# Kernel tuning notes

Measured on AMD Instinct MI355X. Metric: run time of the kernel, lower is better.

Reference implementation:

```python
import jax, jax.numpy as jnp
import numpy as np

# Static config (KITTI PointPillars-style)
B, PB, N = 4, 12000, 32          # batches, pillars per batch, max points per pillar
P = B * PB
NX, NY, NZ, F = 432, 496, 1, 64  # grid and PFN output channels
PX, PY, PZ = 0.16, 0.16, 4.0     # pillar size
XO, YO, ZO = 0.08, -39.6, -1.0   # pillar-center offsets = size/2 + range_min
EPS = 1e-3                        # BatchNorm eps


def setup_inputs() -> dict:
    key = jax.random.key(0)
    ks = jax.random.split(key, 10)
    pillars = jax.random.normal(ks[0], (P, N, 8), jnp.float32)
    # unique BEV cells per batch so the scatter (torch advanced-index assign) is well-defined
    rng = np.random.default_rng(0)
    cs = []
    for b in range(B):
        lin = rng.choice(NY * NX, size=PB, replace=False)
        cs.append(np.stack([np.full(PB, b), np.zeros(PB, np.int64), lin // NX, lin % NX], 1))
    coords = jnp.asarray(np.concatenate(cs, 0), jnp.int32)  # [P,4] = (batch, z, y, x)
    num_points = jax.random.randint(ks[1], (P,), 1, N + 1, jnp.int32)

    def bn_stats(k, f):  # rows: gamma, beta, running_mean, running_var
        k1, k2, k3, k4 = jax.random.split(k, 4)
        return jnp.stack([jax.random.uniform(k1, (f,), jnp.float32, 0.8, 1.2),
                          jax.random.normal(k2, (f,)) * 0.1,
                          jax.random.normal(k3, (f,)) * 0.1,
                          jax.random.uniform(k4, (f,), jnp.float32, 0.5, 1.5)])

    return {
        'pillars': pillars,
        'w1': jax.random.normal(ks[2], (10, F), jnp.float32) * 0.1,
        'bn1': bn_stats(ks[4], F),
        'w2': jax.random.normal(ks[3], (8, F), jnp.float32) * 0.1,
        'bn2': bn_stats(ks[5], F),
        'wf1': jax.random.normal(ks[6], (F,), jnp.float32) * 0.1,
        'wf2': jax.random.normal(ks[7], (F,), jnp.float32) * 0.1,
        'fbn1': bn_stats(ks[8], 1)[:, 0],
        'fbn2': bn_stats(ks[9], 1)[:, 0],
        'coords': coords,
        'num_points': num_points,
    }


def _bn(x, stats):  # x [..., F], stats [4, F] or [4]
    g, b, m, v = stats[0], stats[1], stats[2], stats[3]
    return (x - m) * (g * jax.lax.rsqrt(v + EPS)) + b


def _pfn(x, w, stats):  # x [P, N, C] -> [P, F]: linear + BN(eval) + relu + max over points
    h = jnp.einsum('pnc,cf->pnf', x, w)
    return jax.nn.relu(_bn(h, stats)).max(axis=1)


def _forward(pillars, w1, bn1, w2, bn2, wf1, wf2, fbn1, fbn2, coords, num_points):
    xyz = pillars[:, :, :3]                                   # [P, N, 3]
    # relative xyz to cluster mean
    mean_xyz = xyz.sum(axis=1, keepdims=True) / num_points.astype(jnp.float32)[:, None, None]
    to_cluster = xyz - mean_xyz
    # relative xyz to pillar center; coords cols = (batch, z, y, x)
    cf = coords.astype(jnp.float32)
    center = jnp.stack([cf[:, 3] * PX + XO, cf[:, 2] * PY + YO, cf[:, 1] * PZ + ZO], axis=-1)
    to_center = xyz - center[:, None, :]

    pv_in = jnp.concatenate([pillars[:, :, :4], to_cluster, to_center], axis=-1)  # [P, N, 10]
    f1 = _pfn(pv_in, w1, bn1)      # [P, F] geometric stream
    f2 = _pfn(pillars, w2, bn2)    # [P, F] seg stream (full 8 channels)

    # scatter pillar features to BEV canvas: idx = z + y*nx + x (nz=1 -> z=0)
    lin = coords[:, 1] + coords[:, 2] * NX + coords[:, 3]
    b_idx = coords[:, 0]
    bev1 = jnp.zeros((B, NZ * NY * NX, F), jnp.float32).at[b_idx, lin].set(f1)
    bev2 = jnp.zeros((B, NZ * NY * NX, F), jnp.float32).at[b_idx, lin].set(f2)
    x1 = bev1.reshape(B, NY, NX, F).transpose(0, 3, 1, 2)  # [B, F, NY, NX]
    x2 = bev2.reshape(B, NY, NX, F).transpose(0, 3, 1, 2)

    # attentional fusion: 1x1 conv (no bias) + BN2d(1) per stream, softmax over the 2 weights
    s1 = _bn(jnp.einsum('bfyx,f->byx', x1, wf1), fbn1)
    s2 = _bn(jnp.einsum('bfyx,f->byx', x2, wf2), fbn2)
    aw = jax.nn.softmax(jnp.stack([s1, s2], axis=1), axis=1)  # [B, 2, NY, NX]
    return x1 * aw[:, 0:1] + x2 * aw[:, 1:2]


def reference(pillars, w1, bn1, w2, bn2, wf1, wf2, fbn1, fbn2, coords, num_points):
    return _forward(pillars, w1, bn1, w2, bn2, wf1, wf2, fbn1, fbn2, coords, num_points)
```

## Files before the change

### kernel.cpp

```cpp
#include <hip/hip_runtime.h>
#include <math.h>

#define NXC 432
#define NYC 496
#define CELLS (NYC * NXC)
#define BATCH 4
#define PTOT 48000
#define EPSC 1e-3f
#define TCELLS 128

typedef float f4v    __attribute__((ext_vector_type(4)));
typedef float f32x16 __attribute__((ext_vector_type(16)));
typedef __bf16 bf16x8 __attribute__((ext_vector_type(8)));

__global__ __launch_bounds__(256) void pfe_kernel(
    const float* __restrict__ pillars, const float* __restrict__ w1,
    const float* __restrict__ bn1, const float* __restrict__ w2,
    const float* __restrict__ bn2, const float* __restrict__ wf1,
    const float* __restrict__ wf2, const float* __restrict__ fbn1,
    const float* __restrict__ fbn2, const int* __restrict__ coords,
    const int* __restrict__ num_points, float* __restrict__ comb,
    int* __restrict__ map)
{
    const int tid  = threadIdx.x;
    const int lane = tid & 63;
    const int ln   = lane & 31;
    const bool hi  = lane >= 32;
    const int p = __builtin_amdgcn_readfirstlane(blockIdx.x * 4 + (tid >> 6));
    const float* __restrict__ pl = pillars + (size_t)p * 256;

    const f4v v0 = *(const f4v*)(pl + ln * 8);
    const f4v v1 = *(const f4v*)(pl + ln * 8 + 4);

    float sx = v0.x, sy = v0.y, sz = v0.z;
#pragma unroll
    for (int off = 1; off <= 16; off <<= 1) {
        sx += __shfl_xor(sx, off);
        sy += __shfl_xor(sy, off);
        sz += __shfl_xor(sz, off);
    }
    const float inv_np = 1.0f / (float)num_points[p];
    const float mxm = sx * inv_np, mym = sy * inv_np, mzm = sz * inv_np;

    const int c1 = coords[p * 4 + 1], c2 = coords[p * 4 + 2], c3 = coords[p * 4 + 3];
    const float cx = c3 * 0.16f + 0.08f;
    const float cy = c2 * 0.16f + (-39.6f);
    const float cz = c1 * 4.0f  + (-1.0f);

    float AXc[2], AYc[2], AZc[2], AIc[2], C0c[2];
    float Bc[2][8], C2c[2], WF1c[2], WF2c[2];
#pragma unroll
    for (int i = 0; i < 2; ++i) {
        const int c = ln + i * 32;
        const float s1 = bn1[c] * rsqrtf(bn1[192 + c] + EPSC);
        const float be1 = bn1[64 + c], bm1 = bn1[128 + c];
        const float w10 = w1[c],       w11 = w1[64 + c],  w12 = w1[128 + c];
        const float w13 = w1[192 + c], w14 = w1[256 + c], w15 = w1[320 + c];
        const float w16 = w1[384 + c], w17 = w1[448 + c], w18 = w1[512 + c];
        const float w19 = w1[576 + c];
        AXc[i] = (w10 + w14 + w17) * s1;
        AYc[i] = (w11 + w15 + w18) * s1;
        AZc[i] = (w12 + w16 + w19) * s1;
        AIc[i] = w13 * s1;
        C0c[i] = be1 - bm1 * s1
               - (mxm * w14 + mym * w15 + mzm * w16) * s1
               - (cx * w17 + cy * w18 + cz * w19) * s1;

        const float s2 = bn2[c] * rsqrtf(bn2[192 + c] + EPSC);
#pragma unroll
        for (int k = 0; k < 8; ++k) Bc[i][k] = w2[k * 64 + c] * s2;
        C2c[i] = bn2[64 + c] - bn2[128 + c] * s2;
        WF1c[i] = wf1[c];
        WF2c[i] = wf2[c];
    }

    const float fe0 = v0.x, fe1 = v0.y, fe2 = v0.z, fe3 = v0.w;
    const float fe4 = v1.x, fe5 = v1.y, fe6 = v1.z, fe7 = v1.w;
    bf16x8 a;
    {
        const float f[8] = {fe0, fe1, fe2, fe3, fe4, fe5, fe6, fe7};
#pragma unroll
        for (int e = 0; e < 8; ++e) {
            const __bf16 h = (__bf16)f[e];
            const __bf16 l = (__bf16)(f[e] - (float)h);
            a[e] = hi ? l : h;
        }
    }

    const bf16x8 b0 = {(__bf16)AXc[0], (__bf16)AYc[0], (__bf16)AZc[0], (__bf16)AIc[0],
                       (__bf16)0.f, (__bf16)0.f, (__bf16)0.f, (__bf16)0.f};
    const bf16x8 b1 = {(__bf16)AXc[1], (__bf16)AYc[1], (__bf16)AZc[1], (__bf16)AIc[1],
                       (__bf16)0.f, (__bf16)0.f, (__bf16)0.f, (__bf16)0.f};
    const bf16x8 b2 = {(__bf16)Bc[0][0], (__bf16)Bc[0][1], (__bf16)Bc[0][2], (__bf16)Bc[0][3],
                       (__bf16)Bc[0][4], (__bf16)Bc[0][5], (__bf16)Bc[0][6], (__bf16)Bc[0][7]};
    const bf16x8 b3 = {(__bf16)Bc[1][0], (__bf16)Bc[1][1], (__bf16)Bc[1][2], (__bf16)Bc[1][3],
                       (__bf16)Bc[1][4], (__bf16)Bc[1][5], (__bf16)Bc[1][6], (__bf16)Bc[1][7]};

    f32x16 d0 = {0.f}, d1 = {0.f}, d2 = {0.f}, d3 = {0.f};
    d0 = __builtin_amdgcn_mfma_f32_32x32x16_bf16(a, b0, d0, 0, 0, 0);
    d1 = __builtin_amdgcn_mfma_f32_32x32x16_bf16(a, b1, d1, 0, 0, 0);
    d2 = __builtin_amdgcn_mfma_f32_32x32x16_bf16(a, b2, d2, 0, 0, 0);
    d3 = __builtin_amdgcn_mfma_f32_32x32x16_bf16(a, b3, d3, 0, 0, 0);

    float m0 = d0[0], m1 = d1[0], m2 = d2[0], m3 = d3[0];
#pragma unroll
    for (int r = 1; r < 16; ++r) {
        m0 = fmaxf(m0, d0[r]); m1 = fmaxf(m1, d1[r]);
        m2 = fmaxf(m2, d2[r]); m3 = fmaxf(m3, d3[r]);
    }
    m0 = fmaxf(m0, __shfl_xor(m0, 32));
    m1 = fmaxf(m1, __shfl_xor(m1, 32));
    m2 = fmaxf(m2, __shfl_xor(m2, 32));
    m3 = fmaxf(m3, __shfl_xor(m3, 32));

    const float f1A = fmaxf(m0 + C0c[0], 0.f);
    const float f1B = fmaxf(m1 + C0c[1], 0.f);
    const float f2A = fmaxf(m2 + C2c[0], 0.f);
    const float f2B = fmaxf(m3 + C2c[1], 0.f);

    float dd1 = f1A * WF1c[0] + f1B * WF1c[1];
    float dd2 = f2A * WF2c[0] + f2B * WF2c[1];
#pragma unroll
    for (int off = 1; off <= 16; off <<= 1) {
        dd1 += __shfl_xor(dd1, off);
        dd2 += __shfl_xor(dd2, off);
    }
    const float sc1 = (dd1 - fbn1[2]) * (fbn1[0] * rsqrtf(fbn1[3] + EPSC)) + fbn1[1];
    const float sc2 = (dd2 - fbn2[2]) * (fbn2[0] * rsqrtf(fbn2[3] + EPSC)) + fbn2[1];
    const float a0 = 1.0f / (1.0f + expf(sc2 - sc1));

    if (!hi) {
        comb[p * 64 + ln]      = fmaf(f1A - f2A, a0, f2A);
        comb[p * 64 + 32 + ln] = fmaf(f1B - f2B, a0, f2B);
    }
    if (lane == 0) {
        const int lin = c1 + c2 * NXC + c3;
        map[coords[p * 4 + 0] * CELLS + lin] = p;
    }
}

__global__ __launch_bounds__(256) void emit_kernel(
    const int* __restrict__ map, const float* __restrict__ comb,
    float* __restrict__ out)
{
    __shared__ float lds[64 * 132];
    const int t = threadIdx.x;
    const int gbase = blockIdx.x * TCELLS;

    {
        const int c = t >> 1;
        const int h = (t & 1) * 32;
        const int m = map[gbase + c];
        float* dst = lds + h * 132 + c;
        if (m >= 0) {
            const float* src = comb + (size_t)m * 64 + h;
#pragma unroll
            for (int j = 0; j < 8; j++) {
                const float4 v = *(const float4*)(src + j * 4);
                dst[(j * 4 + 0) * 132] = v.x;
                dst[(j * 4 + 1) * 132] = v.y;
                dst[(j * 4 + 2) * 132] = v.z;
                dst[(j * 4 + 3) * 132] = v.w;
            }
        } else {
#pragma unroll
            for (int j = 0; j < 32; j++) dst[j * 132] = 0.f;
        }
    }
    __syncthreads();

    const int b = gbase / CELLS;
    const int L = gbase - b * CELLS;
    float* obase = out + (size_t)(b * 64) * CELLS + L;
#pragma unroll
    for (int r = 0; r < 8; r++) {
        const int idx = r * 256 + t;
        const int f = idx >> 5;
        const int g = idx & 31;
        const f4v v = *(const f4v*)(lds + f * 132 + g * 4);
        __builtin_nontemporal_store(v, (f4v*)(obase + (size_t)f * CELLS + g * 4));
    }
}

extern "C" void kernel_launch(void* const* d_in, const int* in_sizes, int n_in,
                              void* d_out, int out_size, void* d_ws, size_t ws_size,
                              hipStream_t stream) {
    const float* pillars = (const float*)d_in[0];
    const float* w1      = (const float*)d_in[1];
    const float* bn1     = (const float*)d_in[2];
    const float* w2      = (const float*)d_in[3];
    const float* bn2     = (const float*)d_in[4];
    const float* wf1     = (const float*)d_in[5];
    const float* wf2     = (const float*)d_in[6];
    const float* fbn1    = (const float*)d_in[7];
    const float* fbn2    = (const float*)d_in[8];
    const int*   coords  = (const int*)d_in[9];
    const int*   nump    = (const int*)d_in[10];
    float* out = (float*)d_out;

    int*   map  = (int*)d_ws;
    float* comb = (float*)((char*)d_ws + (size_t)BATCH * CELLS * 4);

    (void)hipMemsetAsync(map, 0xFF, (size_t)BATCH * CELLS * 4, stream);
    pfe_kernel<<<PTOT / 4, 256, 0, stream>>>(pillars, w1, bn1, w2, bn2,
                                             wf1, wf2, fbn1, fbn2,
                                             coords, nump, comb, map);
    emit_kernel<<<(BATCH * CELLS) / TCELLS, 256, 0, stream>>>(map, comb, out);
}
```

Baseline: 89.16 us.

## Precompute folded BN weights once in a table kernel; skip zero-fill LDS writes in emit

A new single-block kernel folds the BatchNorm scale and shift into the PFN weights once per call and stores them as packed bf16 MFMA operands plus float constants in a workspace table. Each pillar wave then loads from this table instead of recomputing rsqrt and many weight products per pillar. The emit kernel stops writing zeros into LDS for empty cells and instead records cell occupancy in shared memory, masking values at store time. This adds an extra kernel launch and a dependency on the table in exchange for less per-pillar arithmetic and fewer LDS writes.

Result: faster. 83.88 us (-5.9%).

```diff
diff --git a/kernel.cpp b/kernel.cpp
--- a/kernel.cpp
+++ b/kernel.cpp
@@ -8,19 +8,71 @@
 #define PTOT 48000
 #define EPSC 1e-3f
 #define TCELLS 128
-
+#define TBL_STRIDE 20
+
+typedef float f2v    __attribute__((ext_vector_type(2)));
 typedef float f4v    __attribute__((ext_vector_type(4)));
 typedef float f32x16 __attribute__((ext_vector_type(16)));
 typedef __bf16 bf16x8 __attribute__((ext_vector_type(8)));
+typedef unsigned int u32x4 __attribute__((ext_vector_type(4)));
+
+__device__ __forceinline__ unsigned int pk_bf16(float a, float b) {
+    __bf16 ha = (__bf16)a, hb = (__bf16)b;
+    unsigned short ua = __builtin_bit_cast(unsigned short, ha);
+    unsigned short ub = __builtin_bit_cast(unsigned short, hb);
+    return ((unsigned int)ub << 16) | ua;
+}
+
+__global__ __launch_bounds__(64) void fold_kernel(
+    const float* __restrict__ w1, const float* __restrict__ bn1,
+    const float* __restrict__ w2, const float* __restrict__ bn2,
+    const float* __restrict__ wf1, const float* __restrict__ wf2,
+    unsigned int* __restrict__ tbl)
+{
+    const int c = threadIdx.x;
+    const float s1 = bn1[c] * rsqrtf(bn1[192 + c] + EPSC);
+    const float w10 = w1[c],       w11 = w1[64 + c],  w12 = w1[128 + c];
+    const float w13 = w1[192 + c], w14 = w1[256 + c], w15 = w1[320 + c];
+    const float w16 = w1[384 + c], w17 = w1[448 + c], w18 = w1[512 + c];
+    const float w19 = w1[576 + c];
+    const float AX = (w10 + w14 + w17) * s1;
+    const float AY = (w11 + w15 + w18) * s1;
+    const float AZ = (w12 + w16 + w19) * s1;
+    const float AI = w13 * s1;
+
+    const float s2 = bn2[c] * rsqrtf(bn2[192 + c] + EPSC);
+    float B[8];
+#pragma unroll
+    for (int k = 0; k < 8; ++k) B[k] = w2[k * 64 + c] * s2;
+
+    unsigned int* t = tbl + c * TBL_STRIDE;
+    t[0] = pk_bf16(AX, AY);
+    t[1] = pk_bf16(AZ, AI);
+    t[2] = 0u;
+    t[3] = 0u;
+    t[4] = pk_bf16(B[0], B[1]);
+    t[5] = pk_bf16(B[2], B[3]);
+    t[6] = pk_bf16(B[4], B[5]);
+    t[7] = pk_bf16(B[6], B[7]);
+    float* tf = (float*)t;
+    tf[8]  = bn1[64 + c] - bn1[128 + c] * s1;
+    tf[9]  = w14 * s1;
+    tf[10] = w15 * s1;
+    tf[11] = w16 * s1;
+    tf[12] = w17 * s1;
+    tf[13] = w18 * s1;
+    tf[14] = w19 * s1;
+    tf[15] = bn2[64 + c] - bn2[128 + c] * s2;
+    tf[16] = wf1[c];
+    tf[17] = wf2[c];
+    tf[18] = 0.f; tf[19] = 0.f;
+}
 
 __global__ __launch_bounds__(256) void pfe_kernel(
-    const float* __restrict__ pillars, const float* __restrict__ w1,
-    const float* __restrict__ bn1, const float* __restrict__ w2,
-    const float* __restrict__ bn2, const float* __restrict__ wf1,
-    const float* __restrict__ wf2, const float* __restrict__ fbn1,
-    const float* __restrict__ fbn2, const int* __restrict__ coords,
-    const int* __restrict__ num_points, float* __restrict__ comb,
-    int* __restrict__ map)
+    const float* __restrict__ pillars, const unsigned int* __restrict__ tbl,
+    const float* __restrict__ fbn1, const float* __restrict__ fbn2,
+    const int* __restrict__ coords, const int* __restrict__ num_points,
+    float* __restrict__ comb, int* __restrict__ map)
 {
     const int tid  = threadIdx.x;
     const int lane = tid & 63;
@@ -47,38 +99,26 @@
     const float cy = c2 * 0.16f + (-39.6f);
     const float cz = c1 * 4.0f  + (-1.0f);
 
-    float AXc[2], AYc[2], AZc[2], AIc[2], C0c[2];
-    float Bc[2][8], C2c[2], WF1c[2], WF2c[2];
+    bf16x8 bfr1[2], bfr2[2];
+    float C0c[2], C2c[2], WF1c[2], WF2c[2];
 #pragma unroll
     for (int i = 0; i < 2; ++i) {
-        const int c = ln + i * 32;
-        const float s1 = bn1[c] * rsqrtf(bn1[192 + c] + EPSC);
-        const float be1 = bn1[64 + c], bm1 = bn1[128 + c];
-        const float w10 = w1[c],       w11 = w1[64 + c],  w12 = w1[128 + c];
-        const float w13 = w1[192 + c], w14 = w1[256 + c], w15 = w1[320 + c];
-        const float w16 = w1[384 + c], w17 = w1[448 + c], w18 = w1[512 + c];
-        const float w19 = w1[576 + c];
-        AXc[i] = (w10 + w14 + w17) * s1;
-        AYc[i] = (w11 + w15 + w18) * s1;
-        AZc[i] = (w12 + w16 + w19) * s1;
-        AIc[i] = w13 * s1;
-        C0c[i] = be1 - bm1 * s1
-               - (mxm * w14 + mym * w15 + mzm * w16) * s1
-               - (cx * w17 + cy * w18 + cz * w19) * s1;
-
-        const float s2 = bn2[c] * rsqrtf(bn2[192 + c] + EPSC);
-#pragma unroll
-        for (int k = 0; k < 8; ++k) Bc[i][k] = w2[k * 64 + c] * s2;
-        C2c[i] = bn2[64 + c] - bn2[128 + c] * s2;
-        WF1c[i] = wf1[c];
-        WF2c[i] = wf2[c];
-    }
-
-    const float fe0 = v0.x, fe1 = v0.y, fe2 = v0.z, fe3 = v0.w;
-    const float fe4 = v1.x, fe5 = v1.y, fe6 = v1.z, fe7 = v1.w;
+        const unsigned int* t = tbl + (ln + i * 32) * TBL_STRIDE;
+        bfr1[i] = __builtin_bit_cast(bf16x8, *(const u32x4*)t);
+        bfr2[i] = __builtin_bit_cast(bf16x8, *(const u32x4*)(t + 4));
+        const f4v k0 = *(const f4v*)(t + 8);
+        const f4v k1 = *(const f4v*)(t + 12);
+        const f2v wfp = *(const f2v*)(t + 16);
+        C0c[i] = k0.x - (mxm * k0.y + mym * k0.z + mzm * k0.w)
+                      - (cx * k1.x + cy * k1.y + cz * k1.z);
+        C2c[i] = k1.w;
+        WF1c[i] = wfp.x;
+        WF2c[i] = wfp.y;
+    }
+
     bf16x8 a;
     {
-        const float f[8] = {fe0, fe1, fe2, fe3, fe4, fe5, fe6, fe7};
+        const float f[8] = {v0.x, v0.y, v0.z, v0.w, v1.x, v1.y, v1.z, v1.w};
 #pragma unroll
         for (int e = 0; e < 8; ++e) {
             const __bf16 h = (__bf16)f[e];
@@ -87,20 +127,11 @@
         }
     }
 
-    const bf16x8 b0 = {(__bf16)AXc[0], (__bf16)AYc[0], (__bf16)AZc[0], (__bf16)AIc[0],
-                       (__bf16)0.f, (__bf16)0.f, (__bf16)0.f, (__bf16)0.f};
-    const bf16x8 b1 = {(__bf16)AXc[1], (__bf16)AYc[1], (__bf16)AZc[1], (__bf16)AIc[1],
-                       (__bf16)0.f, (__bf16)0.f, (__bf16)0.f, (__bf16)0.f};
-    const bf16x8 b2 = {(__bf16)Bc[0][0], (__bf16)Bc[0][1], (__bf16)Bc[0][2], (__bf16)Bc[0][3],
-                       (__bf16)Bc[0][4], (__bf16)Bc[0][5], (__bf16)Bc[0][6], (__bf16)Bc[0][7]};
-    const bf16x8 b3 = {(__bf16)Bc[1][0], (__bf16)Bc[1][1], (__bf16)Bc[1][2], (__bf16)Bc[1][3],
-                       (__bf16)Bc[1][4], (__bf16)Bc[1][5], (__bf16)Bc[1][6], (__bf16)Bc[1][7]};
-
     f32x16 d0 = {0.f}, d1 = {0.f}, d2 = {0.f}, d3 = {0.f};
-    d0 = __builtin_amdgcn_mfma_f32_32x32x16_bf16(a, b0, d0, 0, 0, 0);
-    d1 = __builtin_amdgcn_mfma_f32_32x32x16_bf16(a, b1, d1, 0, 0, 0);
-    d2 = __builtin_amdgcn_mfma_f32_32x32x16_bf16(a, b2, d2, 0, 0, 0);
-    d3 = __builtin_amdgcn_mfma_f32_32x32x16_bf16(a, b3, d3, 0, 0, 0);
+    d0 = __builtin_amdgcn_mfma_f32_32x32x16_bf16(a, bfr1[0], d0, 0, 0, 0);
+    d1 = __builtin_amdgcn_mfma_f32_32x32x16_bf16(a, bfr1[1], d1, 0, 0, 0);
+    d2 = __builtin_amdgcn_mfma_f32_32x32x16_bf16(a, bfr2[0], d2, 0, 0, 0);
+    d3 = __builtin_amdgcn_mfma_f32_32x32x16_bf16(a, bfr2[1], d3, 0, 0, 0);
 
     float m0 = d0[0], m1 = d1[0], m2 = d2[0], m3 = d3[0];
 #pragma unroll
@@ -144,6 +175,7 @@
     float* __restrict__ out)
 {
     __shared__ float lds[64 * 132];
+    __shared__ int mcell[128];
     const int t = threadIdx.x;
     const int gbase = blockIdx.x * TCELLS;
 
@@ -151,9 +183,10 @@
         const int c = t >> 1;
         const int h = (t & 1) * 32;
         const int m = map[gbase + c];
-        float* dst = lds + h * 132 + c;
+        if ((t & 1) == 0) mcell[c] = m;
         if (m >= 0) {
             const float* src = comb + (size_t)m * 64 + h;
+            float* dst = lds + h * 132 + c;
 #pragma unroll
             for (int j = 0; j < 8; j++) {
                 const float4 v = *(const float4*)(src + j * 4);
@@ -162,9 +195,6 @@
                 dst[(j * 4 + 2) * 132] = v.z;
                 dst[(j * 4 + 3) * 132] = v.w;
             }
-        } else {
-#pragma unroll
-            for (int j = 0; j < 32; j++) dst[j * 132] = 0.f;
         }
     }
     __syncthreads();
@@ -177,7 +207,15 @@
         const int idx = r * 256 + t;
         const int f = idx >> 5;
         const int g = idx & 31;
-        const f4v v = *(const f4v*)(lds + f * 132 + g * 4);
+        const int4 mg = *(const int4*)&mcell[g * 4];
+        f4v v = {0.f, 0.f, 0.f, 0.f};
+        if ((mg.x & mg.y & mg.z & mg.w) >= 0) {
+            const f4v w = *(const f4v*)(lds + f * 132 + g * 4);
+            v.x = (mg.x < 0) ? 0.f : w.x;
+            v.y = (mg.y < 0) ? 0.f : w.y;
+            v.z = (mg.z < 0) ? 0.f : w.z;
+            v.w = (mg.w < 0) ? 0.f : w.w;
+        }
         __builtin_nontemporal_store(v, (f4v*)(obase + (size_t)f * CELLS + g * 4));
     }
 }
@@ -200,10 +238,12 @@
 
     int*   map  = (int*)d_ws;
     float* comb = (float*)((char*)d_ws + (size_t)BATCH * CELLS * 4);
+    unsigned int* tbl = (unsigned int*)((char*)d_ws + (size_t)BATCH * CELLS * 4
+                                        + (size_t)PTOT * 64 * 4);
 
     (void)hipMemsetAsync(map, 0xFF, (size_t)BATCH * CELLS * 4, stream);
-    pfe_kernel<<<PTOT / 4, 256, 0, stream>>>(pillars, w1, bn1, w2, bn2,
-                                             wf1, wf2, fbn1, fbn2,
+    fold_kernel<<<1, 64, 0, stream>>>(w1, bn1, w2, bn2, wf1, wf2, tbl);
+    pfe_kernel<<<PTOT / 4, 256, 0, stream>>>(pillars, tbl, fbn1, fbn2,
                                              coords, nump, comb, map);
     emit_kernel<<<(BATCH * CELLS) / TCELLS, 256, 0, stream>>>(map, comb, out);
 }
```
